# Kernel tuning notes

Hardware: AMD Instinct MI355X
Metric: run time of the kernel (lower is better)

Reference implementation:

```python
import jax, jax.numpy as jnp
import numpy as np

B, N, E, H = 8, 2000, 20, 128


def setup_inputs() -> dict:
    key = jax.random.key(0)
    ks = jax.random.split(key, 9)
    s = 1.0 / np.sqrt(H)
    return {
        "x": jax.random.normal(ks[0], (B, N, H), dtype=jnp.float32),
        "e": jax.random.normal(ks[1], (B, N * E, H), dtype=jnp.float32),
        "Wu": jax.random.uniform(ks[2], (H, H), jnp.float32, -s, s),
        "bu": jax.random.uniform(ks[3], (H,), jnp.float32, -s, s),
        "Wv": jax.random.uniform(ks[4], (H, H), jnp.float32, -s, s),
        "bv": jax.random.uniform(ks[5], (H,), jnp.float32, -s, s),
        "We": jax.random.uniform(ks[6], (H, H), jnp.float32, -s, s),
        "be": jax.random.uniform(ks[7], (H,), jnp.float32, -s, s),
        "edge_index": jax.random.randint(ks[8], (B, N * E), 0, N, dtype=jnp.int32),
        "n_edges": E,
    }


def reference(x, e, Wu, bu, Wv, bv, We, be, edge_index, n_edges):
    b, n, h = x.shape
    Ux = x @ Wu + bu                      # [B, N, H] node self-embedding
    Vx = x @ Wv + bv                      # [B, N, H] neighbor embedding
    Ve = e @ We + be                      # [B, N*E, H] edge embedding
    # softmax over the n_edges axis per (node, channel)
    Ve = jax.nn.softmax(Ve.reshape(b, n, n_edges, h), axis=2)
    # gather neighbor features along node axis via edge_index
    Vx_g = jnp.take_along_axis(Vx, edge_index[..., None], axis=1)  # [B, N*E, H]
    to = (Ve * Vx_g.reshape(b, n, n_edges, h)).sum(axis=2)          # [B, N, H]
    return Ux + to
```

## Files before the change

kernel.cpp:

```cpp
#include <hip/hip_runtime.h>

#define B_   8
#define NN   2000
#define EE   20
#define HH   128
#define BN   (B_*NN)
#define NE   (NN*EE)

typedef unsigned short ushort_t;
typedef __bf16 bf16x8 __attribute__((ext_vector_type(8)));
typedef float  f32x4  __attribute__((ext_vector_type(4)));
typedef float  f4     __attribute__((ext_vector_type(4)));
typedef unsigned short us8 __attribute__((ext_vector_type(8)));
typedef unsigned short us4 __attribute__((ext_vector_type(4)));

union FragU { us8 u; bf16x8 b; };

__device__ __forceinline__ float b2f(ushort_t v) {
    union { unsigned int i; float f; } c; c.i = ((unsigned int)v) << 16; return c.f;
}
__device__ __forceinline__ ushort_t f2b(float f) {
    union { float f; unsigned int i; } c; c.f = f;
    unsigned int r = (c.i + 0x7FFFu + ((c.i >> 16) & 1u)) >> 16;
    return (ushort_t)r;
}

__global__ __launch_bounds__(256) void k1_embed(
    const float* __restrict__ x,
    const float* __restrict__ Wu, const float* __restrict__ bu,
    const float* __restrict__ Wv, const float* __restrict__ bv,
    ushort_t* __restrict__ Uxb, ushort_t* __restrict__ Vxb)
{
    const int tid  = threadIdx.x;
    const int lane = tid & 63;
    const int wave = tid >> 6;
    const int wm = wave >> 1, wn = wave & 1;
    const int q  = lane >> 4, ln = lane & 15;
    const int m0 = blockIdx.x * 64;
    const int sel = blockIdx.y;
    const float* W    = sel ? Wv : Wu;
    const float* bias = sel ? bv : bu;
    ushort_t* dst = sel ? Vxb : Uxb;

    FragU af[2][4];
#pragma unroll
    for (int tm = 0; tm < 2; ++tm)
#pragma unroll
        for (int ki = 0; ki < 4; ++ki) {
            const float* p = x + (size_t)(m0 + wm * 32 + tm * 16 + ln) * HH + ki * 32 + q * 8;
            f4 lo = *(const f4*)(p);
            f4 hi = *(const f4*)(p + 4);
            us8 t;
#pragma unroll
            for (int r = 0; r < 4; ++r) { t[r] = f2b(lo[r]); t[r + 4] = f2b(hi[r]); }
            af[tm][ki].u = t;
        }

    FragU bf[4][4];
#pragma unroll
    for (int ki = 0; ki < 4; ++ki)
#pragma unroll
        for (int tn = 0; tn < 4; ++tn) {
            int n = wn * 64 + tn * 16 + ln;
            us8 t;
#pragma unroll
            for (int i = 0; i < 8; ++i) t[i] = f2b(W[(ki * 32 + q * 8 + i) * HH + n]);
            bf[ki][tn].u = t;
        }

    f32x4 acc[2][4];
#pragma unroll
    for (int tm = 0; tm < 2; ++tm)
#pragma unroll
        for (int tn = 0; tn < 4; ++tn) acc[tm][tn] = (f32x4){0.f, 0.f, 0.f, 0.f};

#pragma unroll
    for (int ki = 0; ki < 4; ++ki)
#pragma unroll
        for (int tm = 0; tm < 2; ++tm)
#pragma unroll
            for (int tn = 0; tn < 4; ++tn)
                acc[tm][tn] = __builtin_amdgcn_mfma_f32_16x16x32_bf16(
                    af[tm][ki].b, bf[ki][tn].b, acc[tm][tn], 0, 0, 0);

#pragma unroll
    for (int tn = 0; tn < 4; ++tn) {
        int col = wn * 64 + tn * 16 + ln;
        float bb = bias[col];
#pragma unroll
        for (int tm = 0; tm < 2; ++tm) {
            int rowb = m0 + wm * 32 + tm * 16 + q * 4;
#pragma unroll
            for (int r = 0; r < 4; ++r)
                dst[(size_t)(rowb + r) * HH + col] = f2b(acc[tm][tn][r] + bb);
        }
    }
}

#define ASTR 136
#define CSTR 84

__global__ __launch_bounds__(256, 4) void k2_fused(
    const float* __restrict__ e, const float* __restrict__ We,
    const int* __restrict__ eidx,
    const ushort_t* __restrict__ Uxb, const ushort_t* __restrict__ Vxb,
    float* __restrict__ out)
{
    __shared__ __align__(16) ushort_t smem[11008];
    __shared__ int sidx[80];

    const int tid  = threadIdx.x;
    const int lane = tid & 63;
    const int wave = tid >> 6;
    const int q  = lane >> 4, ln = lane & 15;

    const int b   = blockIdx.y;
    const int nl0 = blockIdx.x * 4;
    const size_t erow0 = (size_t)b * NE + (size_t)nl0 * EE;

    for (int c = tid; c < 80 * 32; c += 256) {
        int row = c >> 5, col = (c & 31) * 4;
        f4 v = *(const f4*)(e + (erow0 + row) * HH + col);
        us4 pk;
#pragma unroll
        for (int r = 0; r < 4; ++r) pk[r] = f2b(v[r]);
        *(us4*)(&smem[row * ASTR + col]) = pk;
    }
    if (tid < 80) sidx[tid] = eidx[erow0 + tid];

    FragU bf[4][2];
#pragma unroll
    for (int ki = 0; ki < 4; ++ki)
#pragma unroll
        for (int tn = 0; tn < 2; ++tn) {
            int n = wave * 32 + tn * 16 + ln;
            us8 t;
#pragma unroll
            for (int i = 0; i < 8; ++i) t[i] = f2b(We[(ki * 32 + q * 8 + i) * HH + n]);
            bf[ki][tn].u = t;
        }

    f32x4 acc[5][2];
#pragma unroll
    for (int tm = 0; tm < 5; ++tm)
#pragma unroll
        for (int tn = 0; tn < 2; ++tn) acc[tm][tn] = (f32x4){0.f, 0.f, 0.f, 0.f};

    __syncthreads();

#pragma unroll
    for (int ki = 0; ki < 4; ++ki) {
        FragU af[5];
#pragma unroll
        for (int tm = 0; tm < 5; ++tm)
            af[tm].u = *(const us8*)(&smem[(tm * 16 + ln) * ASTR + ki * 32 + q * 8]);
#pragma unroll
        for (int tm = 0; tm < 5; ++tm)
#pragma unroll
            for (int tn = 0; tn < 2; ++tn)
                acc[tm][tn] = __builtin_amdgcn_mfma_f32_16x16x32_bf16(
                    af[tm].b, bf[ki][tn].b, acc[tm][tn], 0, 0, 0);
    }

    __syncthreads();

#pragma unroll
    for (int tm = 0; tm < 5; ++tm)
#pragma unroll
        for (int tn = 0; tn < 2; ++tn) {
            int col  = wave * 32 + tn * 16 + ln;
            int rowb = tm * 16 + q * 4;
            us4 pk;
#pragma unroll
            for (int r = 0; r < 4; ++r) pk[r] = f2b(acc[tm][tn][r]);
            *(us4*)(&smem[col * CSTR + rowb]) = pk;
        }

    __syncthreads();

    const int h  = tid & 127;
    const int gp = tid >> 7;
#pragma unroll 1
    for (int j = 0; j < 2; ++j) {
        int g = gp + 2 * j;
        const ushort_t* ctp = &smem[h * CSTR + g * 20];
        float lv[20];
#pragma unroll
        for (int i = 0; i < 5; ++i) {
            us4 v = *(const us4*)(ctp + i * 4);
#pragma unroll
            for (int r = 0; r < 4; ++r) lv[i * 4 + r] = b2f(v[r]);
        }
        float mx = lv[0];
#pragma unroll
        for (int k = 1; k < EE; ++k) mx = fmaxf(mx, lv[k]);

        ushort_t gv[20];
        const int ib = g * 20;
#pragma unroll
        for (int k = 0; k < EE; ++k)
            gv[k] = Vxb[(size_t)(b * NN + sidx[ib + k]) * HH + h];

        float s = 0.f, a = 0.f;
#pragma unroll
        for (int k = 0; k < EE; ++k) {
            float p = __expf(lv[k] - mx);
            s += p;
            a = fmaf(p, b2f(gv[k]), a);
        }
        size_t orow = (size_t)(b * NN + nl0 + g) * HH + h;
        out[orow] = b2f(Uxb[orow]) + a / s;
    }
}

extern "C" void kernel_launch(void* const* d_in, const int* in_sizes, int n_in,
                              void* d_out, int out_size, void* d_ws, size_t ws_size,
                              hipStream_t stream) {
    const float* x  = (const float*)d_in[0];
    const float* e  = (const float*)d_in[1];
    const float* Wu = (const float*)d_in[2];
    const float* bu = (const float*)d_in[3];
    const float* Wv = (const float*)d_in[4];
    const float* bv = (const float*)d_in[5];
    const float* We = (const float*)d_in[6];
    const int*   eidx = (const int*)d_in[8];

    ushort_t* Uxb = (ushort_t*)d_ws;
    ushort_t* Vxb = (ushort_t*)((char*)d_ws + (size_t)BN * HH * 2);
    float*    o   = (float*)d_out;

    k1_embed<<<dim3(250, 2), 256, 0, stream>>>(x, Wu, bu, Wv, bv, Uxb, Vxb);
    k2_fused<<<dim3(500, 8), 256, 0, stream>>>(e, We, eidx, Uxb, Vxb, o);
}
```

Measured before the change: 275.7 us.

## Pre-convert weights to transposed bf16 in a prep kernel and drop a barrier

Adds a prep kernel that converts x to bf16 and writes Wu, Wv and We transposed in bf16. The GEMM kernels can then load MFMA B fragments with contiguous 16-byte loads, replacing strided scalar fp32 loads and per-element conversion that every block repeated. In the fused kernel, the softmax/gather phase is remapped so each wave reads only the smem columns it wrote itself, which lets the last __syncthreads be removed. The cost is an extra kernel launch and an extra pass over x through workspace memory.

```diff
diff --git a/kernel.cpp b/kernel.cpp
--- a/kernel.cpp
+++ b/kernel.cpp
@@ -25,10 +25,43 @@
     return (ushort_t)r;
 }
 
-__global__ __launch_bounds__(256) void k1_embed(
+__global__ __launch_bounds__(256) void k0_prep(
     const float* __restrict__ x,
-    const float* __restrict__ Wu, const float* __restrict__ bu,
-    const float* __restrict__ Wv, const float* __restrict__ bv,
+    const float* __restrict__ Wu, const float* __restrict__ Wv,
+    const float* __restrict__ We,
+    ushort_t* __restrict__ xb,
+    ushort_t* __restrict__ WuT, ushort_t* __restrict__ WvT,
+    ushort_t* __restrict__ WeT)
+{
+    const int bid = blockIdx.x;
+    if (bid < 125) {
+        const size_t base = (size_t)bid * 128 * HH;
+#pragma unroll
+        for (int it = 0; it < 16; ++it) {
+            int c = it * 256 + threadIdx.x;
+            size_t off = base + (size_t)c * 4;
+            f4 v = *(const f4*)(x + off);
+            us4 pk;
+#pragma unroll
+            for (int r = 0; r < 4; ++r) pk[r] = f2b(v[r]);
+            *(us4*)(xb + off) = pk;
+        }
+    } else {
+        const float* W = (bid == 125) ? Wu : (bid == 126) ? Wv : We;
+        ushort_t*   WT = (bid == 125) ? WuT : (bid == 126) ? WvT : WeT;
+#pragma unroll
+        for (int it = 0; it < 64; ++it) {
+            int c = it * 256 + threadIdx.x;
+            int k = c >> 7, n = c & 127;
+            WT[n * HH + k] = f2b(W[c]);
+        }
+    }
+}
+
+__global__ __launch_bounds__(256, 4) void k1_embed(
+    const ushort_t* __restrict__ xb,
+    const ushort_t* __restrict__ WuT, const float* __restrict__ bu,
+    const ushort_t* __restrict__ WvT, const float* __restrict__ bv,
     ushort_t* __restrict__ Uxb, ushort_t* __restrict__ Vxb)
 {
     const int tid  = threadIdx.x;
@@ -38,50 +71,32 @@
     const int q  = lane >> 4, ln = lane & 15;
     const int m0 = blockIdx.x * 64;
     const int sel = blockIdx.y;
-    const float* W    = sel ? Wv : Wu;
-    const float* bias = sel ? bv : bu;
+    const ushort_t* WT   = sel ? WvT : WuT;
+    const float*    bias = sel ? bv : bu;
     ushort_t* dst = sel ? Vxb : Uxb;
 
-    FragU af[2][4];
+    f32x4 acc[2][4];
 #pragma unroll
     for (int tm = 0; tm < 2; ++tm)
 #pragma unroll
-        for (int ki = 0; ki < 4; ++ki) {
-            const float* p = x + (size_t)(m0 + wm * 32 + tm * 16 + ln) * HH + ki * 32 + q * 8;
-            f4 lo = *(const f4*)(p);
-            f4 hi = *(const f4*)(p + 4);
-            us8 t;
-#pragma unroll
-            for (int r = 0; r < 4; ++r) { t[r] = f2b(lo[r]); t[r + 4] = f2b(hi[r]); }
-            af[tm][ki].u = t;
-        }
-
-    FragU bf[4][4];
-#pragma unroll
-    for (int ki = 0; ki < 4; ++ki)
-#pragma unroll
-        for (int tn = 0; tn < 4; ++tn) {
-            int n = wn * 64 + tn * 16 + ln;
-            us8 t;
-#pragma unroll
-            for (int i = 0; i < 8; ++i) t[i] = f2b(W[(ki * 32 + q * 8 + i) * HH + n]);
-            bf[ki][tn].u = t;
-        }
-
-    f32x4 acc[2][4];
-#pragma unroll
-    for (int tm = 0; tm < 2; ++tm)
-#pragma unroll
         for (int tn = 0; tn < 4; ++tn) acc[tm][tn] = (f32x4){0.f, 0.f, 0.f, 0.f};
 
 #pragma unroll
-    for (int ki = 0; ki < 4; ++ki)
+    for (int ki = 0; ki < 4; ++ki) {
+        FragU af[2], bf[4];
+#pragma unroll
+        for (int tm = 0; tm < 2; ++tm)
+            af[tm].u = *(const us8*)(xb + (size_t)(m0 + wm * 32 + tm * 16 + ln) * HH + ki * 32 + q * 8);
+#pragma unroll
+        for (int tn = 0; tn < 4; ++tn)
+            bf[tn].u = *(const us8*)(WT + (size_t)(wn * 64 + tn * 16 + ln) * HH + ki * 32 + q * 8);
 #pragma unroll
         for (int tm = 0; tm < 2; ++tm)
 #pragma unroll
             for (int tn = 0; tn < 4; ++tn)
                 acc[tm][tn] = __builtin_amdgcn_mfma_f32_16x16x32_bf16(
-                    af[tm][ki].b, bf[ki][tn].b, acc[tm][tn], 0, 0, 0);
+                    af[tm].b, bf[tn].b, acc[tm][tn], 0, 0, 0);
+    }
 
 #pragma unroll
     for (int tn = 0; tn < 4; ++tn) {
@@ -101,7 +116,7 @@
 #define CSTR 84
 
 __global__ __launch_bounds__(256, 4) void k2_fused(
-    const float* __restrict__ e, const float* __restrict__ We,
+    const float* __restrict__ e, const ushort_t* __restrict__ WeT,
     const int* __restrict__ eidx,
     const ushort_t* __restrict__ Uxb, const ushort_t* __restrict__ Vxb,
     float* __restrict__ out)
@@ -118,7 +133,9 @@
     const int nl0 = blockIdx.x * 4;
     const size_t erow0 = (size_t)b * NE + (size_t)nl0 * EE;
 
-    for (int c = tid; c < 80 * 32; c += 256) {
+#pragma unroll
+    for (int it = 0; it < 10; ++it) {
+        int c = it * 256 + tid;
         int row = c >> 5, col = (c & 31) * 4;
         f4 v = *(const f4*)(e + (erow0 + row) * HH + col);
         us4 pk;
@@ -132,13 +149,8 @@
 #pragma unroll
     for (int ki = 0; ki < 4; ++ki)
 #pragma unroll
-        for (int tn = 0; tn < 2; ++tn) {
-            int n = wave * 32 + tn * 16 + ln;
-            us8 t;
-#pragma unroll
-            for (int i = 0; i < 8; ++i) t[i] = f2b(We[(ki * 32 + q * 8 + i) * HH + n]);
-            bf[ki][tn].u = t;
-        }
+        for (int tn = 0; tn < 2; ++tn)
+            bf[ki][tn].u = *(const us8*)(WeT + (size_t)(wave * 32 + tn * 16 + ln) * HH + ki * 32 + q * 8);
 
     f32x4 acc[5][2];
 #pragma unroll
@@ -176,13 +188,14 @@
             *(us4*)(&smem[col * CSTR + rowb]) = pk;
         }
 
-    __syncthreads();
-
-    const int h  = tid & 127;
-    const int gp = tid >> 7;
-#pragma unroll 1
+
+    const int hh = lane & 31;
+    const int gh = lane >> 5;
+    const int h  = wave * 32 + hh;
+    const ushort_t* vbase = Vxb + (size_t)b * NN * HH + h;
+#pragma unroll
     for (int j = 0; j < 2; ++j) {
-        int g = gp + 2 * j;
+        int g = gh + 2 * j;
         const ushort_t* ctp = &smem[h * CSTR + g * 20];
         float lv[20];
 #pragma unroll
@@ -199,7 +212,7 @@
         const int ib = g * 20;
 #pragma unroll
         for (int k = 0; k < EE; ++k)
-            gv[k] = Vxb[(size_t)(b * NN + sidx[ib + k]) * HH + h];
+            gv[k] = vbase[(size_t)sidx[ib + k] * HH];
 
         float s = 0.f, a = 0.f;
 #pragma unroll
@@ -225,10 +238,16 @@
     const float* We = (const float*)d_in[6];
     const int*   eidx = (const int*)d_in[8];
 
+    const size_t SZ = (size_t)BN * HH * 2;
     ushort_t* Uxb = (ushort_t*)d_ws;
-    ushort_t* Vxb = (ushort_t*)((char*)d_ws + (size_t)BN * HH * 2);
+    ushort_t* Vxb = (ushort_t*)((char*)d_ws + SZ);
+    ushort_t* xb  = (ushort_t*)((char*)d_ws + 2 * SZ);
+    ushort_t* WuT = (ushort_t*)((char*)d_ws + 3 * SZ);
+    ushort_t* WvT = WuT + HH * HH;
+    ushort_t* WeT = WvT + HH * HH;
     float*    o   = (float*)d_out;
 
-    k1_embed<<<dim3(250, 2), 256, 0, stream>>>(x, Wu, bu, Wv, bv, Uxb, Vxb);
-    k2_fused<<<dim3(500, 8), 256, 0, stream>>>(e, We, eidx, Uxb, Vxb, o);
-}
+    k0_prep<<<dim3(128), 256, 0, stream>>>(x, Wu, Wv, We, xb, WuT, WvT, WeT);
+    k1_embed<<<dim3(250, 2), 256, 0, stream>>>(xb, WuT, bu, WvT, bv, Uxb, Vxb);
+    k2_fused<<<dim3(500, 8), 256, 0, stream>>>(e, WeT, eidx, Uxb, Vxb, o);
+}
```

Result: slower. 283.2 us (+2.7%).
